# Kernel tuning notes

Hardware: AMD Instinct MI355X
Metric: run time of the kernel (lower is better)

Reference implementation:

```python
import jax, jax.numpy as jnp
import numpy as np


def setup_inputs() -> dict:
    key = jax.random.key(0)
    k1, k2, k3 = jax.random.split(key, 3)
    B, C, H, W = 8, 64, 112, 112
    kh, kw = 5, 5
    return {
        "x": jax.random.normal(k1, (B, C, H, W), dtype=jnp.float32),
        "weight": jax.random.normal(k2, (C, kh, kw), dtype=jnp.float32),
        "bias": jax.random.normal(k3, (C,), dtype=jnp.float32),
        "sign": jnp.ones((1,), dtype=jnp.float32),
        "padding": 2,
        "stride": 1,
        "func_type": 1,
        "alpha": 1,
    }


def _morpho(x, weight, bias, sign, padding, stride, func_type, alpha):
    B, C, H, W = x.shape
    kh, kw = weight.shape[-2:]
    ph = pw = padding
    sh = sw = stride
    H2 = (H + 2 * ph - kh) // sh + 1
    W2 = (W + 2 * pw - kw) // sw + 1
    # sign handling: m*sign*x + (1-m)*x == (m*sign + (1-m)) * x, m detached
    m = jax.lax.stop_gradient((jnp.abs(sign) >= 1e-7).astype(x.dtype))
    s = (m * sign + (1.0 - m)).reshape(-1, 1, 1, 1)  # broadcasts over B or is scalar
    xe = s * x
    xp = jnp.pad(xe, ((0, 0), (0, 0), (ph, ph), (pw, pw)))  # zero pad like F.unfold
    # gather sliding-window taps: [B, C, kh*kw, H2, W2]
    patches = jnp.stack(
        [xp[:, :, i : i + sh * H2 : sh, j : j + sw * W2 : sw]
         for i in range(kh) for j in range(kw)],
        axis=2,
    )
    w = weight.reshape(-1, C, kh * kw, 1, 1)  # (1 or B, C, ks, 1, 1)
    y = patches + w
    if func_type == 0:
        y = y.max(axis=2)
    elif func_type == 1:
        prob = jax.nn.softmax(alpha * y, axis=2)
        y = (y * prob).sum(axis=2)
    elif func_type == 2:
        y = jax.scipy.special.logsumexp(alpha * y, axis=2) / alpha
    else:
        raise NotImplementedError
    if bias is not None:
        y = y + bias.reshape(-1, C, 1, 1)
    y = s * y  # un-apply the sign scaling on the output
    return y  # [B, C, H2, W2]


def reference(x, weight, bias, sign, padding, stride, func_type, alpha):
    return _morpho(x, weight, bias, sign, padding, stride, func_type, alpha)
```

## Files before the change

kernel.cpp:

```cpp
#include <hip/hip_runtime.h>
#include <math.h>

typedef float v2f __attribute__((ext_vector_type(2)));

constexpr int B_  = 8;
constexpr int C_  = 64;
constexpr int H_  = 112;
constexpr int W_  = 112;
constexpr int KH  = 5;
constexpr int KW  = 5;
constexpr int PAD = 2;

constexpr int TRT = 16;
constexpr int NT  = H_ / TRT;
constexpr int LRT = TRT + KH - 1;
constexpr int LCP = 118;
constexpr int TPB = 256;
constexpr int SOUT_LD = 116;
constexpr int NINT = LRT * 28;
constexpr int NSTORE = TRT * 28;

__device__ __forceinline__ void block_sync_lds() {
    asm volatile("s_waitcnt lgkmcnt(0)" ::: "memory");
    __builtin_amdgcn_sched_barrier(0);
    __builtin_amdgcn_s_barrier();
}

__global__ __launch_bounds__(TPB)
void morpho_persist(const float* __restrict__ x,
                    const float* __restrict__ weight,
                    const float* __restrict__ bias,
                    const float* __restrict__ sign,
                    const int*   __restrict__ alpha_p,
                    float* __restrict__ out)
{
    __shared__ __align__(16) char  sraw[2 * LRT * LCP * sizeof(v2f)];
    __shared__ __align__(16) float sOut[TRT * SOUT_LD];
    v2f (*sEF)[LRT][LCP] = reinterpret_cast<v2f (*)[LRT][LCP]>(sraw);

    const int plane = blockIdx.x;
    const int c     = plane & (C_ - 1);
    const int tid   = threadIdx.x;

    const float sg   = sign[0];
    const float seff = (fabsf(sg) >= 1e-7f) ? sg : 1.0f;
    const float a    = (float)alpha_p[0];
    const float aK   = a * seff;

    const float* xp = x + (size_t)plane * (H_ * W_);
    float*       op = out + (size_t)plane * (H_ * W_);

    int r_[3], q_[3];
    bool ok_[3];
#pragma unroll
    for (int k = 0; k < 3; ++k) {
        int i  = tid + TPB * k;
        int ic = (i < NINT) ? i : (NINT - 1);
        r_[k] = ic / 28;
        q_[k] = ic - 28 * r_[k];
        ok_[k] = (i < NINT);
    }

    float4 xcur[3], xnxt[3];
#pragma unroll
    for (int k = 0; k < 3; ++k) {
        int grc = min(max(-PAD + r_[k], 0), H_ - 1);
        xcur[k] = *reinterpret_cast<const float4*>(xp + grc * W_ + 4 * q_[k]);
    }

    const float* wp = weight + c * (KH * KW);
    float su[KH * KW], sv[KH * KW];
#pragma unroll
    for (int k = 0; k < KH * KW; ++k) {
        float wv = wp[k];
        float u  = __expf(a * wv);
        su[k] = u;
        sv[k] = wv * u;
    }
    const float sb = seff * bias[c];

    const int ty = tid >> 4;
    const int tx = tid & 15;
    const int c0 = tx * 7;

    for (int t = 0; t < NT; ++t) {
        const int row0 = t * TRT - PAD;
        v2f (*buf)[LCP] = sEF[t & 1];

#pragma unroll
        for (int k = 0; k < 3; ++k) {
            if (ok_[k]) {
                int gr = row0 + r_[k];
                bool ok = (gr >= 0) && (gr < H_);
                float4 v = xcur[k];
                float e0 = ok ? __expf(aK * v.x) : 1.0f;
                float e1 = ok ? __expf(aK * v.y) : 1.0f;
                float e2 = ok ? __expf(aK * v.z) : 1.0f;
                float e3 = ok ? __expf(aK * v.w) : 1.0f;
                float f0 = ok ? (seff * v.x) * e0 : 0.0f;
                float f1 = ok ? (seff * v.y) * e1 : 0.0f;
                float f2 = ok ? (seff * v.z) * e2 : 0.0f;
                float f3 = ok ? (seff * v.w) * e3 : 0.0f;
                float4* dst = reinterpret_cast<float4*>(&buf[r_[k]][2 + 4 * q_[k]]);
                dst[0] = make_float4(e0, f0, e1, f1);
                dst[1] = make_float4(e2, f2, e3, f3);
            }
        }
        if (tid < 2 * LRT) {
            int r  = tid >> 1;
            int fi = (tid & 1) ? 114 : 0;
            *reinterpret_cast<float4*>(&buf[r][fi]) = make_float4(1.0f, 0.0f, 1.0f, 0.0f);
        }

        if (t + 1 < NT) {
            const int nrow0 = (t + 1) * TRT - PAD;
#pragma unroll
            for (int k = 0; k < 3; ++k) {
                int grc = min(max(nrow0 + r_[k], 0), H_ - 1);
                xnxt[k] = *reinterpret_cast<const float4*>(xp + grc * W_ + 4 * q_[k]);
            }
        }
        block_sync_lds();

        v2f   acc[7];
        float nm2[7];
#pragma unroll
        for (int o = 0; o < 7; ++o) { acc[o] = (v2f){0.0f, 0.0f}; nm2[o] = 0.0f; }

#pragma unroll
        for (int rr = 0; rr < KH; ++rr) {
            v2f ew[11];
#pragma unroll
            for (int jj = 0; jj < 11; ++jj) ew[jj] = buf[ty + rr][c0 + jj];
#pragma unroll
            for (int j = 0; j < KW; ++j) {
                const float u  = su[rr * 5 + j];
                const v2f   u2 = (v2f){u, u};
                const float v  = sv[rr * 5 + j];
#pragma unroll
                for (int o = 0; o < 7; ++o) {
                    acc[o] = __builtin_elementwise_fma(u2, ew[o + j], acc[o]);
                    nm2[o] = fmaf(v, ew[o + j].x, nm2[o]);
                }
            }
        }
#pragma unroll
        for (int o = 0; o < 7; ++o) {
            float Z  = acc[o].x;
            float Nm = acc[o].y + nm2[o];
            sOut[ty * SOUT_LD + c0 + o] = fmaf(seff * Nm, __builtin_amdgcn_rcpf(Z), sb);
        }
        block_sync_lds();

        float* tb = op + (size_t)(t * TRT) * W_;
#pragma unroll
        for (int k = 0; k < 2; ++k) {
            int i = tid + TPB * k;
            if (i < NSTORE) {
                int r = i / 28;
                int q = i - 28 * r;
                *reinterpret_cast<float4*>(tb + r * W_ + 4 * q) =
                    *reinterpret_cast<const float4*>(&sOut[r * SOUT_LD + 4 * q]);
            }
        }

#pragma unroll
        for (int k = 0; k < 3; ++k) xcur[k] = xnxt[k];
    }
}

extern "C" void kernel_launch(void* const* d_in, const int* in_sizes, int n_in,
                              void* d_out, int out_size, void* d_ws, size_t ws_size,
                              hipStream_t stream) {
    const float* x      = (const float*)d_in[0];
    const float* weight = (const float*)d_in[1];
    const float* bias   = (const float*)d_in[2];
    const float* sign   = (const float*)d_in[3];
    const int*   alpha  = (const int*)d_in[7];
    float* out = (float*)d_out;

    dim3 grid(B_ * C_);
    morpho_persist<<<grid, TPB, 0, stream>>>(x, weight, bias, sign, alpha, out);
}
```

Measured before the change: 24.72 us.

## Software-pipeline tile staging and store outputs directly from registers

Restructures the per-plane loop so the exp/LDS staging of tile t+1 runs after computing tile t, with global loads issued two tiles ahead. The shared output staging buffer is dropped and each thread writes its 7 outputs straight to global memory. This leaves one barrier per tile instead of two and frees LDS. Launch bounds also request 4 blocks per CU. The trade-off is that the direct stores are 7 scalar writes per thread, narrower and less coalesced than the float4 stores they replace.

```diff
diff --git a/kernel.cpp b/kernel.cpp
--- a/kernel.cpp
+++ b/kernel.cpp
@@ -16,9 +16,7 @@
 constexpr int LRT = TRT + KH - 1;
 constexpr int LCP = 118;
 constexpr int TPB = 256;
-constexpr int SOUT_LD = 116;
 constexpr int NINT = LRT * 28;
-constexpr int NSTORE = TRT * 28;
 
 __device__ __forceinline__ void block_sync_lds() {
     asm volatile("s_waitcnt lgkmcnt(0)" ::: "memory");
@@ -26,16 +24,15 @@
     __builtin_amdgcn_s_barrier();
 }
 
-__global__ __launch_bounds__(TPB)
-void morpho_persist(const float* __restrict__ x,
-                    const float* __restrict__ weight,
-                    const float* __restrict__ bias,
-                    const float* __restrict__ sign,
-                    const int*   __restrict__ alpha_p,
-                    float* __restrict__ out)
+__global__ __launch_bounds__(TPB, 4)
+void morpho_pipe(const float* __restrict__ x,
+                 const float* __restrict__ weight,
+                 const float* __restrict__ bias,
+                 const float* __restrict__ sign,
+                 const int*   __restrict__ alpha_p,
+                 float* __restrict__ out)
 {
-    __shared__ __align__(16) char  sraw[2 * LRT * LCP * sizeof(v2f)];
-    __shared__ __align__(16) float sOut[TRT * SOUT_LD];
+    __shared__ __align__(16) char sraw[2 * LRT * LCP * sizeof(v2f)];
     v2f (*sEF)[LRT][LCP] = reinterpret_cast<v2f (*)[LRT][LCP]>(sraw);
 
     const int plane = blockIdx.x;
@@ -61,11 +58,11 @@
         ok_[k] = (i < NINT);
     }
 
-    float4 xcur[3], xnxt[3];
+    float4 xc[3];
 #pragma unroll
     for (int k = 0; k < 3; ++k) {
         int grc = min(max(-PAD + r_[k], 0), H_ - 1);
-        xcur[k] = *reinterpret_cast<const float4*>(xp + grc * W_ + 4 * q_[k]);
+        xc[k] = *reinterpret_cast<const float4*>(xp + grc * W_ + 4 * q_[k]);
     }
 
     const float* wp = weight + c * (KH * KW);
@@ -83,16 +80,14 @@
     const int tx = tid & 15;
     const int c0 = tx * 7;
 
-    for (int t = 0; t < NT; ++t) {
-        const int row0 = t * TRT - PAD;
-        v2f (*buf)[LCP] = sEF[t & 1];
-
+    {
+        v2f (*buf)[LCP] = sEF[0];
 #pragma unroll
         for (int k = 0; k < 3; ++k) {
             if (ok_[k]) {
-                int gr = row0 + r_[k];
+                int gr = -PAD + r_[k];
                 bool ok = (gr >= 0) && (gr < H_);
-                float4 v = xcur[k];
+                float4 v = xc[k];
                 float e0 = ok ? __expf(aK * v.x) : 1.0f;
                 float e1 = ok ? __expf(aK * v.y) : 1.0f;
                 float e2 = ok ? __expf(aK * v.z) : 1.0f;
@@ -111,16 +106,16 @@
             int fi = (tid & 1) ? 114 : 0;
             *reinterpret_cast<float4*>(&buf[r][fi]) = make_float4(1.0f, 0.0f, 1.0f, 0.0f);
         }
-
-        if (t + 1 < NT) {
-            const int nrow0 = (t + 1) * TRT - PAD;
-#pragma unroll
-            for (int k = 0; k < 3; ++k) {
-                int grc = min(max(nrow0 + r_[k], 0), H_ - 1);
-                xnxt[k] = *reinterpret_cast<const float4*>(xp + grc * W_ + 4 * q_[k]);
-            }
-        }
-        block_sync_lds();
+#pragma unroll
+        for (int k = 0; k < 3; ++k) {
+            int grc = min(max(TRT - PAD + r_[k], 0), H_ - 1);
+            xc[k] = *reinterpret_cast<const float4*>(xp + grc * W_ + 4 * q_[k]);
+        }
+    }
+    block_sync_lds();
+
+    for (int t = 0; t < NT; ++t) {
+        v2f (*buf)[LCP] = sEF[t & 1];
 
         v2f   acc[7];
         float nm2[7];
@@ -144,28 +139,55 @@
                 }
             }
         }
-#pragma unroll
-        for (int o = 0; o < 7; ++o) {
-            float Z  = acc[o].x;
-            float Nm = acc[o].y + nm2[o];
-            sOut[ty * SOUT_LD + c0 + o] = fmaf(seff * Nm, __builtin_amdgcn_rcpf(Z), sb);
-        }
+        {
+            float* orow = op + (size_t)(t * TRT + ty) * W_ + c0;
+#pragma unroll
+            for (int o = 0; o < 7; ++o) {
+                float Z  = acc[o].x;
+                float Nm = acc[o].y + nm2[o];
+                orow[o] = fmaf(seff * Nm, __builtin_amdgcn_rcpf(Z), sb);
+            }
+        }
+
+        if (t + 1 < NT) {
+            v2f (*nbuf)[LCP] = sEF[(t + 1) & 1];
+            const int nrow0 = (t + 1) * TRT - PAD;
+#pragma unroll
+            for (int k = 0; k < 3; ++k) {
+                if (ok_[k]) {
+                    int gr = nrow0 + r_[k];
+                    bool ok = (gr >= 0) && (gr < H_);
+                    float4 v = xc[k];
+                    float e0 = ok ? __expf(aK * v.x) : 1.0f;
+                    float e1 = ok ? __expf(aK * v.y) : 1.0f;
+                    float e2 = ok ? __expf(aK * v.z) : 1.0f;
+                    float e3 = ok ? __expf(aK * v.w) : 1.0f;
+                    float f0 = ok ? (seff * v.x) * e0 : 0.0f;
+                    float f1 = ok ? (seff * v.y) * e1 : 0.0f;
+                    float f2 = ok ? (seff * v.z) * e2 : 0.0f;
+                    float f3 = ok ? (seff * v.w) * e3 : 0.0f;
+                    float4* dst = reinterpret_cast<float4*>(&nbuf[r_[k]][2 + 4 * q_[k]]);
+                    dst[0] = make_float4(e0, f0, e1, f1);
+                    dst[1] = make_float4(e2, f2, e3, f3);
+                }
+            }
+            if (tid < 2 * LRT) {
+                int r  = tid >> 1;
+                int fi = (tid & 1) ? 114 : 0;
+                *reinterpret_cast<float4*>(&nbuf[r][fi]) = make_float4(1.0f, 0.0f, 1.0f, 0.0f);
+            }
+        }
+
+        if (t + 2 < NT) {
+            const int lrow0 = (t + 2) * TRT - PAD;
+#pragma unroll
+            for (int k = 0; k < 3; ++k) {
+                int grc = min(max(lrow0 + r_[k], 0), H_ - 1);
+                xc[k] = *reinterpret_cast<const float4*>(xp + grc * W_ + 4 * q_[k]);
+            }
+        }
+
         block_sync_lds();
-
-        float* tb = op + (size_t)(t * TRT) * W_;
-#pragma unroll
-        for (int k = 0; k < 2; ++k) {
-            int i = tid + TPB * k;
-            if (i < NSTORE) {
-                int r = i / 28;
-                int q = i - 28 * r;
-                *reinterpret_cast<float4*>(tb + r * W_ + 4 * q) =
-                    *reinterpret_cast<const float4*>(&sOut[r * SOUT_LD + 4 * q]);
-            }
-        }
-
-#pragma unroll
-        for (int k = 0; k < 3; ++k) xcur[k] = xnxt[k];
     }
 }
 
@@ -180,5 +202,5 @@
     float* out = (float*)d_out;
 
     dim3 grid(B_ * C_);
-    morpho_persist<<<grid, TPB, 0, stream>>>(x, weight, bias, sign, alpha, out);
+    morpho_pipe<<<grid, TPB, 0, stream>>>(x, weight, bias, sign, alpha, out);
 }
```

Result: slower. 85.06 us (+244.1%).

## Split each plane across two blocks and store outputs directly without LDS staging

Applied to the files above, without the earlier changes.

Each (batch, channel) plane is now handled by two blocks, one for row tiles 0-3 and one for tiles 4-6, so the grid doubles to expose more parallelism across CUs. The output staging buffer in shared memory and its extra barrier are removed, and each thread writes its 7 consecutive outputs straight to global memory. The direct stores are narrow, strided scalar writes rather than coalesced float4 stores, and the split is uneven. Halo rows are also loaded and exponentiated twice at the split boundary.

```diff
diff --git a/kernel.cpp b/kernel.cpp
--- a/kernel.cpp
+++ b/kernel.cpp
@@ -16,9 +16,7 @@
 constexpr int LRT = TRT + KH - 1;
 constexpr int LCP = 118;
 constexpr int TPB = 256;
-constexpr int SOUT_LD = 116;
 constexpr int NINT = LRT * 28;
-constexpr int NSTORE = TRT * 28;
 
 __device__ __forceinline__ void block_sync_lds() {
     asm volatile("s_waitcnt lgkmcnt(0)" ::: "memory");
@@ -27,20 +25,24 @@
 }
 
 __global__ __launch_bounds__(TPB)
-void morpho_persist(const float* __restrict__ x,
-                    const float* __restrict__ weight,
-                    const float* __restrict__ bias,
-                    const float* __restrict__ sign,
-                    const int*   __restrict__ alpha_p,
-                    float* __restrict__ out)
+void morpho_half(const float* __restrict__ x,
+                 const float* __restrict__ weight,
+                 const float* __restrict__ bias,
+                 const float* __restrict__ sign,
+                 const int*   __restrict__ alpha_p,
+                 float* __restrict__ out)
 {
-    __shared__ __align__(16) char  sraw[2 * LRT * LCP * sizeof(v2f)];
-    __shared__ __align__(16) float sOut[TRT * SOUT_LD];
+    __shared__ __align__(16) char sraw[2 * LRT * LCP * sizeof(v2f)];
     v2f (*sEF)[LRT][LCP] = reinterpret_cast<v2f (*)[LRT][LCP]>(sraw);
 
-    const int plane = blockIdx.x;
+    const int bid   = blockIdx.x;
+    const int plane = bid >> 1;
+    const int half  = bid & 1;
     const int c     = plane & (C_ - 1);
     const int tid   = threadIdx.x;
+
+    const int t0 = half * 4;
+    const int t1 = half ? NT : 4;
 
     const float sg   = sign[0];
     const float seff = (fabsf(sg) >= 1e-7f) ? sg : 1.0f;
@@ -61,11 +63,11 @@
         ok_[k] = (i < NINT);
     }
 
-    float4 xcur[3], xnxt[3];
+    float4 xc[3], xn[3];
 #pragma unroll
     for (int k = 0; k < 3; ++k) {
-        int grc = min(max(-PAD + r_[k], 0), H_ - 1);
-        xcur[k] = *reinterpret_cast<const float4*>(xp + grc * W_ + 4 * q_[k]);
+        int grc = min(max(t0 * TRT - PAD + r_[k], 0), H_ - 1);
+        xc[k] = *reinterpret_cast<const float4*>(xp + grc * W_ + 4 * q_[k]);
     }
 
     const float* wp = weight + c * (KH * KW);
@@ -83,16 +85,16 @@
     const int tx = tid & 15;
     const int c0 = tx * 7;
 
-    for (int t = 0; t < NT; ++t) {
+    for (int t = t0; t < t1; ++t) {
+        v2f (*buf)[LCP] = sEF[t & 1];
         const int row0 = t * TRT - PAD;
-        v2f (*buf)[LCP] = sEF[t & 1];
 
 #pragma unroll
         for (int k = 0; k < 3; ++k) {
             if (ok_[k]) {
                 int gr = row0 + r_[k];
                 bool ok = (gr >= 0) && (gr < H_);
-                float4 v = xcur[k];
+                float4 v = xc[k];
                 float e0 = ok ? __expf(aK * v.x) : 1.0f;
                 float e1 = ok ? __expf(aK * v.y) : 1.0f;
                 float e2 = ok ? __expf(aK * v.z) : 1.0f;
@@ -112,14 +114,15 @@
             *reinterpret_cast<float4*>(&buf[r][fi]) = make_float4(1.0f, 0.0f, 1.0f, 0.0f);
         }
 
-        if (t + 1 < NT) {
+        if (t + 1 < t1) {
             const int nrow0 = (t + 1) * TRT - PAD;
 #pragma unroll
             for (int k = 0; k < 3; ++k) {
                 int grc = min(max(nrow0 + r_[k], 0), H_ - 1);
-                xnxt[k] = *reinterpret_cast<const float4*>(xp + grc * W_ + 4 * q_[k]);
+                xn[k] = *reinterpret_cast<const float4*>(xp + grc * W_ + 4 * q_[k]);
             }
         }
+
         block_sync_lds();
 
         v2f   acc[7];
@@ -144,28 +147,18 @@
                 }
             }
         }
+        {
+            float* orow = op + (size_t)(t * TRT + ty) * W_ + c0;
 #pragma unroll
-        for (int o = 0; o < 7; ++o) {
-            float Z  = acc[o].x;
-            float Nm = acc[o].y + nm2[o];
-            sOut[ty * SOUT_LD + c0 + o] = fmaf(seff * Nm, __builtin_amdgcn_rcpf(Z), sb);
-        }
-        block_sync_lds();
-
-        float* tb = op + (size_t)(t * TRT) * W_;
-#pragma unroll
-        for (int k = 0; k < 2; ++k) {
-            int i = tid + TPB * k;
-            if (i < NSTORE) {
-                int r = i / 28;
-                int q = i - 28 * r;
-                *reinterpret_cast<float4*>(tb + r * W_ + 4 * q) =
-                    *reinterpret_cast<const float4*>(&sOut[r * SOUT_LD + 4 * q]);
+            for (int o = 0; o < 7; ++o) {
+                float Z  = acc[o].x;
+                float Nm = acc[o].y + nm2[o];
+                orow[o] = fmaf(seff * Nm, __builtin_amdgcn_rcpf(Z), sb);
             }
         }
 
 #pragma unroll
-        for (int k = 0; k < 3; ++k) xcur[k] = xnxt[k];
+        for (int k = 0; k < 3; ++k) xc[k] = xn[k];
     }
 }
 
@@ -179,6 +172,6 @@
     const int*   alpha  = (const int*)d_in[7];
     float* out = (float*)d_out;
 
-    dim3 grid(B_ * C_);
-    morpho_persist<<<grid, TPB, 0, stream>>>(x, weight, bias, sign, alpha, out);
+    dim3 grid(B_ * C_ * 2);
+    morpho_half<<<grid, TPB, 0, stream>>>(x, weight, bias, sign, alpha, out);
 }
```

Result: slower. 26.35 us (+6.6%).
